# Optimization experiments

Measured on AMD Instinct MI355X. Metric: run time of the kernel, lower is better.

## Reference

```python
import jax, jax.numpy as jnp
import numpy as np
from jax.ops import segment_sum

NUM_NODES = 100000
NUM_GRAPHS = 256


def gcn_conv(x, src, dst, W, b, num_nodes):
    """PyG GCNConv: add self-loops, symmetric deg^-1/2 normalization,
    out = scatter_add(norm * (xW)[src]) + b."""
    h = x @ W  # [N, H]
    loop = jnp.arange(num_nodes, dtype=src.dtype)
    s = jnp.concatenate([src, loop])
    d = jnp.concatenate([dst, loop])
    deg = segment_sum(jnp.ones_like(d, dtype=h.dtype), d, num_segments=num_nodes)
    dinv = jnp.where(deg > 0, jax.lax.rsqrt(deg), 0.0)
    norm = dinv[s] * dinv[d]  # [E+N]
    msg = h[s] * norm[:, None]
    return segment_sum(msg, d, num_segments=num_nodes) + b


def global_mean_pool(x, batch, num_graphs):
    summed = segment_sum(x, batch, num_segments=num_graphs)
    cnt = segment_sum(jnp.ones_like(batch, dtype=x.dtype), batch, num_segments=num_graphs)
    return summed / jnp.maximum(cnt, 1.0)[:, None]


def setup_inputs() -> dict:
    key = jax.random.key(0)
    ks = jax.random.split(key, 8)
    N, E, F_in, H = NUM_NODES, 3200000, 128, 64
    x = jax.random.normal(ks[0], (N, F_in), dtype=jnp.float32)
    edge_index = jax.random.randint(ks[1], (2, E), 0, N, dtype=jnp.int64)
    batch = jnp.sort(jax.random.randint(ks[2], (N,), 0, NUM_GRAPHS, dtype=jnp.int64))
    def glorot(k, shape):
        fan = shape[0] + shape[1]
        return jax.random.uniform(k, shape, jnp.float32, -1.0, 1.0) * np.sqrt(6.0 / fan)
    return {
        "x": x, "edge_index": edge_index, "batch": batch,
        "W1": glorot(ks[3], (F_in, H)), "b1": jnp.zeros((H,), jnp.float32),
        "W2": glorot(ks[4], (H, H)),   "b2": jnp.zeros((H,), jnp.float32),
        "W3": glorot(ks[5], (H, H)),   "b3": jnp.zeros((H,), jnp.float32),
        "Wl": glorot(ks[6], (H, 2)),   "bl": jnp.zeros((2,), jnp.float32),
    }


def reference(x, edge_index, batch, W1, b1, W2, b2, W3, b3, Wl, bl):
    src, dst = edge_index[0], edge_index[1]
    # Dropout acts as identity in eval mode; reference is deterministic.
    h = jax.nn.relu(gcn_conv(x, src, dst, W1, b1, NUM_NODES))
    h = jax.nn.relu(gcn_conv(h, src, dst, W2, b2, NUM_NODES))
    h = jax.nn.relu(gcn_conv(h, src, dst, W3, b3, NUM_NODES))
    g = global_mean_pool(h, batch, NUM_GRAPHS)  # [G, H]
    return g @ Wl + bl  # [G, 2]
```

## Files before the change

kernel.cpp:

```cpp
#include <hip/hip_runtime.h>
#include <hip/hip_bf16.h>
#include <cstdint>
#include <cstddef>

static constexpr int N_NODES = 100000;
static constexpr int N_GRAPHS = 256;
static constexpr int HF = 64;

#define SCAN_T 256
#define SCAN_E 8
#define SCAN_CHUNK (SCAN_T * SCAN_E)

#define BSHIFT 9
#define BNODES 512
#define ECHUNK 16384
#define SRCBITS 17

typedef unsigned short u16;
typedef unsigned int u32;

__global__ void scan1_k(const int* __restrict__ in, int* __restrict__ out,
                        int* __restrict__ sums, int n) {
    __shared__ int lds[SCAN_T];
    int t = threadIdx.x;
    int base = blockIdx.x * SCAN_CHUNK + t * SCAN_E;
    int v[SCAN_E];
    int s = 0;
#pragma unroll
    for (int i = 0; i < SCAN_E; ++i) {
        int idx = base + i;
        int x = (idx < n) ? in[idx] : 0;
        v[i] = s; s += x;
    }
    lds[t] = s; __syncthreads();
    for (int off = 1; off < SCAN_T; off <<= 1) {
        int a = (t >= off) ? lds[t - off] : 0;
        __syncthreads();
        lds[t] += a;
        __syncthreads();
    }
    int excl = (t == 0) ? 0 : lds[t - 1];
    if (t == SCAN_T - 1) sums[blockIdx.x] = lds[SCAN_T - 1];
#pragma unroll
    for (int i = 0; i < SCAN_E; ++i) {
        int idx = base + i;
        if (idx < n) out[idx] = excl + v[i];
    }
}

__global__ void scan2_k(int* __restrict__ sums, int nb) {
    __shared__ int lds[SCAN_T];
    int t = threadIdx.x;
    lds[t] = (t < nb) ? sums[t] : 0;
    __syncthreads();
    for (int off = 1; off < SCAN_T; off <<= 1) {
        int a = (t >= off) ? lds[t - off] : 0;
        __syncthreads();
        lds[t] += a;
        __syncthreads();
    }
    int excl = (t == 0) ? 0 : lds[t - 1];
    if (t < nb) sums[t] = excl;
}

__global__ void scan3_k(int* __restrict__ out, const int* __restrict__ sums, int n) {
    int idx = blockIdx.x * blockDim.x + threadIdx.x;
    if (idx < n) out[idx] += sums[idx / SCAN_CHUNK];
}

__global__ void bhist_k(const int* __restrict__ dst, int* __restrict__ cnt,
                        int E, int nblk, int NB) {
    __shared__ int c[256];
    int t = threadIdx.x;
    c[t] = 0;
    __syncthreads();
    int base = blockIdx.x * ECHUNK;
    for (int i = t; i < ECHUNK; i += 256) {
        int e = base + i;
        if (e >= E) break;
        atomicAdd(&c[dst[e] >> BSHIFT], 1);
    }
    __syncthreads();
    if (t < NB) cnt[t * nblk + blockIdx.x] = c[t];
}

__global__ void scatter_k(const int* __restrict__ src, const int* __restrict__ dst,
                          const int* __restrict__ scn, int* __restrict__ es,
                          int E, int nblk, int NB) {
    __shared__ int offs[256];
    int t = threadIdx.x;
    if (t < NB) offs[t] = scn[t * nblk + blockIdx.x];
    __syncthreads();
    int base = blockIdx.x * ECHUNK;
    for (int i = t; i < ECHUNK; i += 256) {
        int e = base + i;
        if (e >= E) break;
        int d = dst[e];
        int b = d >> BSHIFT;
        int p = atomicAdd(&offs[b], 1);
        es[p] = ((d & (BNODES - 1)) << SRCBITS) | src[e];
    }
}

__global__ void fill2_k(const int* __restrict__ es, const int* __restrict__ scn,
                        int* __restrict__ rowp, int* __restrict__ deg,
                        float* __restrict__ dinv, int* __restrict__ col,
                        int E, int nblk, int NB, int N) {
    __shared__ int ldeg[BNODES];
    __shared__ int rp[BNODES];
    __shared__ int ps[256];
    int b = blockIdx.x, t = threadIdx.x;
    int ebase = scn[b * nblk];
    int eend = (b + 1 < NB) ? scn[(b + 1) * nblk] : E;
    int d0 = b << BSHIFT;
    int nd = min(BNODES, N - d0);
    ldeg[t] = 0; ldeg[t + 256] = 0;
    __syncthreads();
    for (int e = ebase + t; e < eend; e += 256) atomicAdd(&ldeg[((u32)es[e]) >> SRCBITS], 1);
    __syncthreads();
    int a0 = ldeg[2 * t], a1 = ldeg[2 * t + 1];
    ps[t] = a0 + a1;
    __syncthreads();
    for (int off = 1; off < 256; off <<= 1) {
        int v = (t >= off) ? ps[t - off] : 0;
        __syncthreads();
        ps[t] += v;
        __syncthreads();
    }
    int ex = (t == 0) ? 0 : ps[t - 1];
    rp[2 * t] = ex;
    rp[2 * t + 1] = ex + a0;
    __syncthreads();
    for (int i = t; i < nd; i += 256) {
        int d = d0 + i;
        rowp[d] = ebase + rp[i];
        int dg = ldeg[i];
        deg[d] = dg;
        dinv[d] = rsqrtf((float)(dg + 1));
    }
    __syncthreads();
    ldeg[t] = 0; ldeg[t + 256] = 0;
    __syncthreads();
    for (int e = ebase + t; e < eend; e += 256) {
        u32 w = (u32)es[e];
        int li = w >> SRCBITS;
        int p = atomicAdd(&ldeg[li], 1);
        col[ebase + rp[li] + p] = (int)(w & ((1u << SRCBITS) - 1));
    }
}

__global__ void wtrans_k(const float* __restrict__ W, float4* __restrict__ W4, int total) {
    int idx = blockIdx.x * blockDim.x + threadIdx.x;
    if (idx >= total) return;
    int k4 = idx >> 6, c = idx & 63;
    W4[idx] = make_float4(W[(4 * k4 + 0) * HF + c], W[(4 * k4 + 1) * HF + c],
                          W[(4 * k4 + 2) * HF + c], W[(4 * k4 + 3) * HF + c]);
}

template <int K>
__global__ __launch_bounds__(256, 4) void gemm4_k(const float* __restrict__ in,
                                                  const float4* __restrict__ W4,
                                                  const float* __restrict__ dinv,
                                                  __hip_bfloat16* __restrict__ u, int n) {
    __shared__ float4 Wl[16 * HF];
    __shared__ float4 Xl[64 * 17];
    int t = threadIdx.x;
    int wave = t >> 6, lane = t & 63;
    int rb = blockIdx.x * 64;
    float acc[16];
#pragma unroll
    for (int i = 0; i < 16; ++i) acc[i] = 0.f;
    constexpr int NC = K / 64;
#pragma unroll 1
    for (int kc = 0; kc < NC; ++kc) {
        const float4* Wc = W4 + kc * 16 * HF;
#pragma unroll 1
        for (int i = t; i < 16 * HF; i += 256) Wl[i] = Wc[i];
        {
            int r = t >> 4, q = t & 15;
#pragma unroll 1
            for (int i = 0; i < 4; ++i) {
                int row = r + i * 16;
                int gr = rb + row;
                float4 v = (gr < n)
                    ? *(const float4*)(in + (size_t)gr * K + kc * 64 + q * 4)
                    : make_float4(0.f, 0.f, 0.f, 0.f);
                Xl[row * 17 + q] = v;
            }
        }
        __syncthreads();
        int r0 = wave * 16;
#pragma unroll 1
        for (int k4 = 0; k4 < 16; ++k4) {
            float4 w = Wl[k4 * HF + lane];
#pragma unroll
            for (int r = 0; r < 16; ++r) {
                float4 v = Xl[(r0 + r) * 17 + k4];
                acc[r] = fmaf(v.x, w.x, fmaf(v.y, w.y, fmaf(v.z, w.z, fmaf(v.w, w.w, acc[r]))));
            }
        }
        __syncthreads();
    }
#pragma unroll 1
    for (int r = 0; r < 16; ++r) {
        int row = rb + wave * 16 + r;
        if (row < n) u[(size_t)row * HF + lane] = __float2bfloat16(acc[r] * dinv[row]);
    }
}

__global__ __launch_bounds__(256) void agg2_k(const u32* __restrict__ u,
                                              const int* __restrict__ col,
                                              const int* __restrict__ rowp,
                                              const int* __restrict__ deg,
                                              const float* __restrict__ dinv,
                                              const float* __restrict__ bias,
                                              float* __restrict__ out, int n) {
    int t = threadIdx.x;
    int wave = t >> 6, lane = t & 63;
    int sl = lane & 31;
    int v = blockIdx.x * 8 + wave * 2 + (lane >> 5);
    if (v >= n) return;
    u32 q = u[(size_t)v * 32 + sl];
    float ax = __uint_as_float(q << 16);
    float ay = __uint_as_float(q & 0xffff0000u);
    int start = rowp[v];
    int nE = deg[v];
    for (int e = 0; e < nE;) {
        int m = min(32, nE - e);
        int c = (sl < m) ? col[start + e + sl] : 0;
        int i = 0;
        for (; i + 4 <= m; i += 4) {
            int s0 = __shfl(c, i, 32),     s1 = __shfl(c, i + 1, 32);
            int s2 = __shfl(c, i + 2, 32), s3 = __shfl(c, i + 3, 32);
            u32 q0 = u[(size_t)s0 * 32 + sl];
            u32 q1 = u[(size_t)s1 * 32 + sl];
            u32 q2 = u[(size_t)s2 * 32 + sl];
            u32 q3 = u[(size_t)s3 * 32 + sl];
            ax += __uint_as_float(q0 << 16);         ay += __uint_as_float(q0 & 0xffff0000u);
            ax += __uint_as_float(q1 << 16);         ay += __uint_as_float(q1 & 0xffff0000u);
            ax += __uint_as_float(q2 << 16);         ay += __uint_as_float(q2 & 0xffff0000u);
            ax += __uint_as_float(q3 << 16);         ay += __uint_as_float(q3 & 0xffff0000u);
        }
        for (; i < m; ++i) {
            int s = __shfl(c, i, 32);
            u32 qq = u[(size_t)s * 32 + sl];
            ax += __uint_as_float(qq << 16);
            ay += __uint_as_float(qq & 0xffff0000u);
        }
        e += m;
    }
    float dv = dinv[v];
    float2 o;
    o.x = fmaxf(fmaf(ax, dv, bias[2 * sl]), 0.f);
    o.y = fmaxf(fmaf(ay, dv, bias[2 * sl + 1]), 0.f);
    ((float2*)out)[(size_t)v * 32 + sl] = o;
}

__device__ __forceinline__ int lower_bound_i(const int* a, int n, int key) {
    int lo = 0, hi = n;
    while (lo < hi) { int mid = (lo + hi) >> 1; if (a[mid] < key) lo = mid + 1; else hi = mid; }
    return lo;
}

__global__ void pool_head_k(const float* __restrict__ h, const int* __restrict__ batch,
                            const float* __restrict__ Wl, const float* __restrict__ bl,
                            float* __restrict__ out, int n) {
    __shared__ float ssum[4][HF];
    __shared__ float smean[HF];
    int g = blockIdx.x;
    int wave = threadIdx.x >> 6, lane = threadIdx.x & 63;
    int start = lower_bound_i(batch, n, g);
    int end = lower_bound_i(batch, n, g + 1);
    float acc = 0.f;
    for (int v = start + wave; v < end; v += 4) acc += h[(size_t)v * HF + lane];
    ssum[wave][lane] = acc;
    __syncthreads();
    if (wave == 0) {
        float s = ssum[0][lane] + ssum[1][lane] + ssum[2][lane] + ssum[3][lane];
        float cnt = (float)(end - start);
        smean[lane] = s / fmaxf(cnt, 1.f);
    }
    __syncthreads();
    if (threadIdx.x < 2) {
        float o = bl[threadIdx.x];
        for (int j = 0; j < HF; ++j) o += smean[j] * Wl[j * 2 + threadIdx.x];
        out[g * 2 + threadIdx.x] = o;
    }
}

extern "C" void kernel_launch(void* const* d_in, const int* in_sizes, int n_in,
                              void* d_out, int out_size, void* d_ws, size_t ws_size,
                              hipStream_t stream) {
    const float* x     = (const float*)d_in[0];
    const int*   ei    = (const int*)d_in[1];
    const int*   batch = (const int*)d_in[2];
    const float* W1 = (const float*)d_in[3];
    const float* b1 = (const float*)d_in[4];
    const float* W2 = (const float*)d_in[5];
    const float* b2 = (const float*)d_in[6];
    const float* W3 = (const float*)d_in[7];
    const float* b3 = (const float*)d_in[8];
    const float* Wl = (const float*)d_in[9];
    const float* bl = (const float*)d_in[10];
    float* outp = (float*)d_out;

    const int N = N_NODES;
    const int E = in_sizes[1] / 2;
    const int NB = (N + BNODES - 1) >> BSHIFT;
    const int NBLK = (E + ECHUNK - 1) / ECHUNK;
    const int M = NB * NBLK;

    char* ws = (char*)d_ws;
    size_t off = 0;
    auto alloc = [&](size_t bytes) {
        void* p = ws + off;
        off = (off + bytes + 255) & ~size_t(255);
        return p;
    };
    size_t ubytes = (size_t)N * HF * 2;
    if ((size_t)E * 4 > ubytes) ubytes = (size_t)E * 4;
    float*  P    = (float*)alloc((size_t)N * HF * 4);
    void*   Uv   = alloc(ubytes);
    int*    colA = (int*)alloc((size_t)E * 4);
    int*    deg  = (int*)alloc((size_t)N * 4);
    float*  dinv = (float*)alloc((size_t)N * 4);
    int*    rowp = (int*)alloc((size_t)N * 4);
    int*    cnt  = (int*)alloc((size_t)M * 4);
    int*    scn  = (int*)alloc((size_t)M * 4);
    int*    sums = (int*)alloc(1024);
    float4* W4_1 = (float4*)alloc((size_t)(128 / 4) * HF * 16);
    float4* W4_2 = (float4*)alloc((size_t)(64 / 4) * HF * 16);
    float4* W4_3 = (float4*)alloc((size_t)(64 / 4) * HF * 16);
    __hip_bfloat16* U = (__hip_bfloat16*)Uv;
    u32* U32 = (u32*)Uv;
    int* es  = (int*)Uv;
    (void)ws_size; (void)n_in; (void)out_size;

    const int* src = ei;
    const int* dst = ei + E;

    bhist_k<<<NBLK, 256, 0, stream>>>(dst, cnt, E, NBLK, NB);
    int nb = (M + SCAN_CHUNK - 1) / SCAN_CHUNK;
    scan1_k<<<nb, SCAN_T, 0, stream>>>(cnt, scn, sums, M);
    scan2_k<<<1, SCAN_T, 0, stream>>>(sums, nb);
    scan3_k<<<(M + 255) / 256, 256, 0, stream>>>(scn, sums, M);
    scatter_k<<<NBLK, 256, 0, stream>>>(src, dst, scn, es, E, NBLK, NB);
    fill2_k<<<NB, 256, 0, stream>>>(es, scn, rowp, deg, dinv, colA, E, NBLK, NB, N);

    wtrans_k<<<(32 * HF + 255) / 256, 256, 0, stream>>>(W1, W4_1, 32 * HF);
    wtrans_k<<<(16 * HF + 255) / 256, 256, 0, stream>>>(W2, W4_2, 16 * HF);
    wtrans_k<<<(16 * HF + 255) / 256, 256, 0, stream>>>(W3, W4_3, 16 * HF);

    int gRow8  = (N + 7) / 8;
    int gRow64 = (N + 63) / 64;
    gemm4_k<128><<<gRow64, 256, 0, stream>>>(x, W4_1, dinv, U, N);
    agg2_k<<<gRow8, 256, 0, stream>>>(U32, colA, rowp, deg, dinv, b1, P, N);
    gemm4_k<64><<<gRow64, 256, 0, stream>>>(P, W4_2, dinv, U, N);
    agg2_k<<<gRow8, 256, 0, stream>>>(U32, colA, rowp, deg, dinv, b2, P, N);
    gemm4_k<64><<<gRow64, 256, 0, stream>>>(P, W4_3, dinv, U, N);
    agg2_k<<<gRow8, 256, 0, stream>>>(U32, colA, rowp, deg, dinv, b3, P, N);

    pool_head_k<<<N_GRAPHS, 256, 0, stream>>>(P, batch, Wl, bl, outp, N);
}
```

Baseline: 425.6 us.

## Shrink edge chunks, widen CSR fill blocks, unroll gather loop by eight

Edge chunk size for the histogram and scatter passes drops from 16384 to 4096, giving four times as many blocks for more parallelism across CUs but a larger count matrix to scan. The CSR fill kernel now runs 512 threads with one node per thread, which simplifies the scan and doubles threads for the edge loops. The aggregation gather loop is unrolled to eight independent loads to keep more memory requests in flight, at some register cost. The scan scratch buffer grows to hold the larger number of partial sums.

```diff
diff --git a/kernel.cpp b/kernel.cpp
--- a/kernel.cpp
+++ b/kernel.cpp
@@ -13,7 +13,7 @@
 
 #define BSHIFT 9
 #define BNODES 512
-#define ECHUNK 16384
+#define ECHUNK 4096
 #define SRCBITS 17
 
 typedef unsigned short u16;
@@ -75,11 +75,8 @@
     c[t] = 0;
     __syncthreads();
     int base = blockIdx.x * ECHUNK;
-    for (int i = t; i < ECHUNK; i += 256) {
-        int e = base + i;
-        if (e >= E) break;
-        atomicAdd(&c[dst[e] >> BSHIFT], 1);
-    }
+    int m = min(ECHUNK, E - base);
+    for (int i = t; i < m; i += 256) atomicAdd(&c[dst[base + i] >> BSHIFT], 1);
     __syncthreads();
     if (t < NB) cnt[t * nblk + blockIdx.x] = c[t];
 }
@@ -92,9 +89,9 @@
     if (t < NB) offs[t] = scn[t * nblk + blockIdx.x];
     __syncthreads();
     int base = blockIdx.x * ECHUNK;
-    for (int i = t; i < ECHUNK; i += 256) {
+    int m = min(ECHUNK, E - base);
+    for (int i = t; i < m; i += 256) {
         int e = base + i;
-        if (e >= E) break;
         int d = dst[e];
         int b = d >> BSHIFT;
         int p = atomicAdd(&offs[b], 1);
@@ -102,46 +99,43 @@
     }
 }
 
-__global__ void fill2_k(const int* __restrict__ es, const int* __restrict__ scn,
-                        int* __restrict__ rowp, int* __restrict__ deg,
-                        float* __restrict__ dinv, int* __restrict__ col,
-                        int E, int nblk, int NB, int N) {
+__global__ __launch_bounds__(512) void fill2_k(const int* __restrict__ es,
+                                               const int* __restrict__ scn,
+                                               int* __restrict__ rowp, int* __restrict__ deg,
+                                               float* __restrict__ dinv, int* __restrict__ col,
+                                               int E, int nblk, int NB, int N) {
     __shared__ int ldeg[BNODES];
     __shared__ int rp[BNODES];
-    __shared__ int ps[256];
+    __shared__ int tmp[BNODES];
     int b = blockIdx.x, t = threadIdx.x;
     int ebase = scn[b * nblk];
     int eend = (b + 1 < NB) ? scn[(b + 1) * nblk] : E;
     int d0 = b << BSHIFT;
     int nd = min(BNODES, N - d0);
-    ldeg[t] = 0; ldeg[t + 256] = 0;
-    __syncthreads();
-    for (int e = ebase + t; e < eend; e += 256) atomicAdd(&ldeg[((u32)es[e]) >> SRCBITS], 1);
-    __syncthreads();
-    int a0 = ldeg[2 * t], a1 = ldeg[2 * t + 1];
-    ps[t] = a0 + a1;
-    __syncthreads();
-    for (int off = 1; off < 256; off <<= 1) {
-        int v = (t >= off) ? ps[t - off] : 0;
-        __syncthreads();
-        ps[t] += v;
-        __syncthreads();
-    }
-    int ex = (t == 0) ? 0 : ps[t - 1];
-    rp[2 * t] = ex;
-    rp[2 * t + 1] = ex + a0;
-    __syncthreads();
-    for (int i = t; i < nd; i += 256) {
-        int d = d0 + i;
-        rowp[d] = ebase + rp[i];
-        int dg = ldeg[i];
-        deg[d] = dg;
-        dinv[d] = rsqrtf((float)(dg + 1));
-    }
-    __syncthreads();
-    ldeg[t] = 0; ldeg[t + 256] = 0;
-    __syncthreads();
-    for (int e = ebase + t; e < eend; e += 256) {
+    ldeg[t] = 0;
+    __syncthreads();
+    for (int e = ebase + t; e < eend; e += 512) atomicAdd(&ldeg[((u32)es[e]) >> SRCBITS], 1);
+    __syncthreads();
+    int a = ldeg[t];
+    tmp[t] = a;
+    __syncthreads();
+    for (int off = 1; off < BNODES; off <<= 1) {
+        int v = (t >= off) ? tmp[t - off] : 0;
+        __syncthreads();
+        tmp[t] += v;
+        __syncthreads();
+    }
+    rp[t] = tmp[t] - a;
+    __syncthreads();
+    if (t < nd) {
+        int d = d0 + t;
+        rowp[d] = ebase + rp[t];
+        deg[d] = a;
+        dinv[d] = rsqrtf((float)(a + 1));
+    }
+    ldeg[t] = 0;
+    __syncthreads();
+    for (int e = ebase + t; e < eend; e += 512) {
         u32 w = (u32)es[e];
         int li = w >> SRCBITS;
         int p = atomicAdd(&ldeg[li], 1);
@@ -229,17 +223,27 @@
         int m = min(32, nE - e);
         int c = (sl < m) ? col[start + e + sl] : 0;
         int i = 0;
-        for (; i + 4 <= m; i += 4) {
+        for (; i + 8 <= m; i += 8) {
             int s0 = __shfl(c, i, 32),     s1 = __shfl(c, i + 1, 32);
             int s2 = __shfl(c, i + 2, 32), s3 = __shfl(c, i + 3, 32);
+            int s4 = __shfl(c, i + 4, 32), s5 = __shfl(c, i + 5, 32);
+            int s6 = __shfl(c, i + 6, 32), s7 = __shfl(c, i + 7, 32);
             u32 q0 = u[(size_t)s0 * 32 + sl];
             u32 q1 = u[(size_t)s1 * 32 + sl];
             u32 q2 = u[(size_t)s2 * 32 + sl];
             u32 q3 = u[(size_t)s3 * 32 + sl];
-            ax += __uint_as_float(q0 << 16);         ay += __uint_as_float(q0 & 0xffff0000u);
-            ax += __uint_as_float(q1 << 16);         ay += __uint_as_float(q1 & 0xffff0000u);
-            ax += __uint_as_float(q2 << 16);         ay += __uint_as_float(q2 & 0xffff0000u);
-            ax += __uint_as_float(q3 << 16);         ay += __uint_as_float(q3 & 0xffff0000u);
+            u32 q4 = u[(size_t)s4 * 32 + sl];
+            u32 q5 = u[(size_t)s5 * 32 + sl];
+            u32 q6 = u[(size_t)s6 * 32 + sl];
+            u32 q7 = u[(size_t)s7 * 32 + sl];
+            ax += __uint_as_float(q0 << 16);  ay += __uint_as_float(q0 & 0xffff0000u);
+            ax += __uint_as_float(q1 << 16);  ay += __uint_as_float(q1 & 0xffff0000u);
+            ax += __uint_as_float(q2 << 16);  ay += __uint_as_float(q2 & 0xffff0000u);
+            ax += __uint_as_float(q3 << 16);  ay += __uint_as_float(q3 & 0xffff0000u);
+            ax += __uint_as_float(q4 << 16);  ay += __uint_as_float(q4 & 0xffff0000u);
+            ax += __uint_as_float(q5 << 16);  ay += __uint_as_float(q5 & 0xffff0000u);
+            ax += __uint_as_float(q6 << 16);  ay += __uint_as_float(q6 & 0xffff0000u);
+            ax += __uint_as_float(q7 << 16);  ay += __uint_as_float(q7 & 0xffff0000u);
         }
         for (; i < m; ++i) {
             int s = __shfl(c, i, 32);
@@ -327,7 +331,7 @@
     int*    rowp = (int*)alloc((size_t)N * 4);
     int*    cnt  = (int*)alloc((size_t)M * 4);
     int*    scn  = (int*)alloc((size_t)M * 4);
-    int*    sums = (int*)alloc(1024);
+    int*    sums = (int*)alloc(4096);
     float4* W4_1 = (float4*)alloc((size_t)(128 / 4) * HF * 16);
     float4* W4_2 = (float4*)alloc((size_t)(64 / 4) * HF * 16);
     float4* W4_3 = (float4*)alloc((size_t)(64 / 4) * HF * 16);
@@ -345,7 +349,7 @@
     scan2_k<<<1, SCAN_T, 0, stream>>>(sums, nb);
     scan3_k<<<(M + 255) / 256, 256, 0, stream>>>(scn, sums, M);
     scatter_k<<<NBLK, 256, 0, stream>>>(src, dst, scn, es, E, NBLK, NB);
-    fill2_k<<<NB, 256, 0, stream>>>(es, scn, rowp, deg, dinv, colA, E, NBLK, NB, N);
+    fill2_k<<<NB, 512, 0, stream>>>(es, scn, rowp, deg, dinv, colA, E, NBLK, NB, N);
 
     wtrans_k<<<(32 * HF + 255) / 256, 256, 0, stream>>>(W1, W4_1, 32 * HF);
     wtrans_k<<<(16 * HF + 255) / 256, 256, 0, stream>>>(W2, W4_2, 16 * HF);
```

Measured after the change: 385.2 us. 9.5% less time.
